# Performance work log

Hardware: AMD Instinct MI355X
Metric: run time of the kernel (lower is better)

Reference implementation:

```python
import jax, jax.numpy as jnp
import numpy as np

ALPHA = 0.1
B, T, D = 32, 1024, 384


def _build_alive(T):
    # Expert j (1-indexed) is created at time j with lifetime 2^(ctz(j)+2)+1.
    def lifetime(j):
        k = (j & -j).bit_length() - 1
        return 2 ** (k + 2) + 1

    sets = [[j for j in range(1, t + 1) if t < j + lifetime(j)]
            for t in range(1, T + 1)]
    K = max(len(s) for s in sets)
    # pad with sentinel index T (the extra never-consumed expert slot)
    idx = np.full((T, K), T, dtype=np.int32)
    mask = np.zeros((T, K), dtype=np.float32)
    for t0, s in enumerate(sets):
        for i, j in enumerate(s):
            idx[t0, i] = j - 1  # 0-indexed expert slot
            mask[t0, i] = 1.0
    return idx, mask


def setup_inputs() -> dict:
    key = jax.random.key(0)
    kx, kw, kb = jax.random.split(key, 3)
    n_exp = T + 1
    x = jax.random.normal(kx, (B, T, D), dtype=jnp.float32)
    # stand-in STULayer = Linear(D, D) per expert
    W = jax.random.normal(kw, (n_exp, D, D), dtype=jnp.float32) / np.float32(np.sqrt(D))
    b = jax.random.normal(kb, (n_exp, D), dtype=jnp.float32) * 0.02
    idx, mask = _build_alive(T)
    return {"x": x, "W": W, "b": b,
            "alive_idx": jnp.asarray(idx), "alive_mask": jnp.asarray(mask)}


def reference(x, W, b, alive_idx, alive_mask):
    Bb, Tt, Dd = x.shape
    n_exp = W.shape[0]
    # initial pool: 1 expert with weight 1
    p0 = jnp.zeros((n_exp,), x.dtype).at[0].set(1.0)
    new_idx = jnp.arange(1, Tt + 1, dtype=jnp.int32)      # slot of expert created at step t
    t_f = jnp.arange(1, Tt + 1, dtype=x.dtype)            # p[new] = 1/t

    def step(p, inp):
        x_t, idx, mask, ni, tf = inp          # x_t: [B,D]; idx,mask: [K]
        Wg = W[idx]                            # [K,D,D]
        bg = b[idx]                            # [K,D]
        outs = jnp.einsum('bd,kde->kbe', x_t, Wg) + bg[:, None, :]  # [K,B,D]
        p_a = p[idx] * mask                    # weights of alive experts
        w = p_a / jnp.sum(p_a)                 # normalized (torch keeps them pre-normalized)
        y_t = jnp.einsum('k,kbe->be', w, outs)
        # soft cross-entropy of expert outputs against x_t (ChunkedCrossEntropyLoss stand-in)
        tgt = jax.nn.softmax(x_t, axis=-1)                       # [B,D]
        logp = jax.nn.log_softmax(outs, axis=-1)                 # [K,B,D]
        loss = -jnp.mean(jnp.sum(tgt[None, :, :] * logp, axis=-1), axis=-1)  # [K]
        loss = jax.lax.stop_gradient(loss)     # torch uses .item() => detached
        # multiplicative weight update, normalize over alive set
        p_upd = p_a * jnp.exp(-ALPHA * loss) * mask
        p_upd = p_upd / jnp.sum(p_upd)
        p = p.at[idx].set(jnp.where(mask > 0, p_upd, p[idx]))
        # spawn new expert with weight 1/t (renormalization deferred to use time)
        p = p.at[ni].set(1.0 / tf)
        return p, y_t

    xs = (jnp.swapaxes(x, 0, 1), alive_idx, alive_mask, new_idx, t_f)
    _, ys = jax.lax.scan(step, p0, xs)        # ys: [T,B,D]
    return jnp.swapaxes(ys, 0, 1)
```

## Files before the change

### kernel.cpp

```cpp
#include <hip/hip_runtime.h>

#define TT 1024
#define BB 32
#define DD 384
#define NE 1025
#define ALPHA_ 0.1f
#define TC 4
#define KSTEP 64
#define NKS 6
#define MROWS 128
#define PADK 72
#define NTHR 512

typedef __attribute__((ext_vector_type(8))) short short8;
typedef __attribute__((ext_vector_type(8))) unsigned short ushort8;
typedef __attribute__((ext_vector_type(4))) float f32x4;

__device__ __forceinline__ unsigned short f2bf(float f) {
    unsigned int u = __float_as_uint(f);
    unsigned int r = u + 0x7fffu + ((u >> 16) & 1u);
    return (unsigned short)(r >> 16);
}

__device__ __host__ __forceinline__ int chunks_of(int j, int* Lout) {
    int k = __builtin_ctz(j);
    int life = (1 << (k + 2)) + 1;
    int jend = j + life - 1; if (jend > TT) jend = TT;
    int L = jend - j + 1;
    *Lout = L;
    return (L + TC - 1) / TC;
}

__device__ __forceinline__ void gl16(const void* g, void* l) {
    __builtin_amdgcn_global_load_lds(
        (const __attribute__((address_space(1))) void*)g,
        (__attribute__((address_space(3))) void*)l, 16, 0, 0);
}

__device__ __forceinline__ float dppsum32(float v) {
    float t;
    t = __int_as_float(__builtin_amdgcn_update_dpp(0, __float_as_int(v), 0x111, 0xf, 0xf, true)); v += t;
    t = __int_as_float(__builtin_amdgcn_update_dpp(0, __float_as_int(v), 0x112, 0xf, 0xf, true)); v += t;
    t = __int_as_float(__builtin_amdgcn_update_dpp(0, __float_as_int(v), 0x114, 0xf, 0xf, true)); v += t;
    t = __int_as_float(__builtin_amdgcn_update_dpp(0, __float_as_int(v), 0x118, 0xf, 0xf, true)); v += t;
    t = __int_as_float(__builtin_amdgcn_update_dpp(0, __float_as_int(v), 0x142, 0xf, 0xf, true)); v += t;
    return __int_as_float(__builtin_amdgcn_readlane(__float_as_int(v), 31));
}

__global__ void setup_all(int* __restrict__ table, int* __restrict__ pref,
                          short* __restrict__ perm16,
                          const int* __restrict__ aidx, const float* __restrict__ amask,
                          int K) {
    __shared__ int sc[1024];
    int b = blockIdx.x, t = threadIdx.x;
    if (b == 0) {
        int j = t + 1;
        int L; int nc = chunks_of(j, &L);
        int start = 0;
        for (int jp = 1; jp < j; ++jp) { int Lp; start += chunks_of(jp, &Lp); }
        for (int c = 0; c < nc; ++c) {
            int cnt = L - c * TC; if (cnt > TC) cnt = TC;
            int* e = table + 3 * (start + c);
            e[0] = j - 1;
            e[1] = (j - 1) + c * TC;
            e[2] = cnt;
        }
    } else if (b == 1) {
        int c = 0;
        for (int kk = 0; kk < K; ++kk) c += (amask[t * K + kk] > 0.f) ? 1 : 0;
        sc[t] = c;
        __syncthreads();
        for (int off = 1; off < 1024; off <<= 1) {
            int v = (t >= off) ? sc[t - off] : 0;
            __syncthreads();
            sc[t] += v;
            __syncthreads();
        }
        if (t == 0) pref[0] = 0;
        pref[t + 1] = sc[t];
    } else {
        int t0 = b - 2;
        int l = t;
        if (l < 32) {
            short enc = 63;
            if (t0 >= 1 && t0 <= TT - 1 && l < K && amask[t0 * K + l] > 0.f) {
                int sp = aidx[t0 * K + l];
                if (sp == t0) enc = (short)(-sp);
                else {
                    for (int kk = 0; kk < K; ++kk)
                        if (aidx[(t0 - 1) * K + kk] == sp) { enc = (short)kk; break; }
                }
            }
            perm16[t0 * 32 + l] = enc;
        }
    }
}

__global__ __launch_bounds__(512)
void conv_w2(const float* __restrict__ W, unsigned short* __restrict__ Wperm) {
    int db = blockIdx.x;
    int j  = blockIdx.y;
    int tid = threadIdx.x, l = tid & 63, w8 = tid >> 6;
    const float* Wj = W + (size_t)j * (DD * DD)
                        + (size_t)(db * 32 + (l >> 4) * 8) * DD + (l & 15);
#pragma unroll
    for (int it = 0; it < 3; ++it) {
        int eblk = it * 8 + w8;
        const float* src = Wj + eblk * 16;
        ushort8 h;
#pragma unroll
        for (int k = 0; k < 8; ++k) h[k] = f2bf(src[(size_t)k * DD]);
        *(ushort8*)&Wperm[(((size_t)j * 12 + db) * 24 + eblk) * 512 + l * 8] = h;
    }
}

__global__ __launch_bounds__(512)
void conv_x2(const float* __restrict__ x, unsigned short* __restrict__ xperm) {
    int t = blockIdx.x;
    int tid = threadIdx.x, l = tid & 63, w8 = tid >> 6;
#pragma unroll
    for (int it = 0; it < 3; ++it) {
        int T = it * 8 + w8;
        int bb = T / 12, db = T - bb * 12;
        const float* src = x + ((size_t)(bb * 16 + (l & 15)) * TT + t) * DD
                             + db * 32 + (l >> 4) * 8;
        float4 f0 = *(const float4*)src;
        float4 f1 = *(const float4*)(src + 4);
        ushort8 h;
        h[0] = f2bf(f0.x); h[1] = f2bf(f0.y); h[2] = f2bf(f0.z); h[3] = f2bf(f0.w);
        h[4] = f2bf(f1.x); h[5] = f2bf(f1.y); h[6] = f2bf(f1.z); h[7] = f2bf(f1.w);
        *(ushort8*)&xperm[(size_t)t * 12288 + T * 512 + l * 8] = h;
    }
}

__global__ void conv_tgt(const float* __restrict__ x, unsigned short* __restrict__ tgtbf) {
    __shared__ unsigned short sL[8 * 384];
    int tid = threadIdx.x;
    int wid = tid >> 6, lane = tid & 63;
    size_t row = (size_t)blockIdx.x * 8 + wid;
    const float* xr = x + row * DD;
    float v[6]; float m = -1e30f;
#pragma unroll
    for (int i = 0; i < 6; ++i) { v[i] = xr[lane + 64 * i]; m = fmaxf(m, v[i]); }
#pragma unroll
    for (int d = 1; d < 64; d <<= 1) m = fmaxf(m, __shfl_xor(m, d));
    float s = 0.f;
#pragma unroll
    for (int i = 0; i < 6; ++i) { v[i] = __expf(v[i] - m); s += v[i]; }
#pragma unroll
    for (int d = 1; d < 64; d <<= 1) s += __shfl_xor(s, d);
    float rz = 1.0f / s;
#pragma unroll
    for (int i = 0; i < 6; ++i) sL[wid * 384 + lane + 64 * i] = f2bf(v[i] * rz);
    __syncthreads();
    unsigned int* dst = (unsigned int*)(tgtbf + (size_t)blockIdx.x * 8 * 384);
    const unsigned int* s32 = (const unsigned int*)sL;
#pragma unroll
    for (int i = 0; i < 3; ++i) dst[i * 512 + tid] = s32[i * 512 + tid];
}

__global__ __launch_bounds__(1024)
void gemmA(const unsigned short* __restrict__ xperm,
           const unsigned short* __restrict__ Wperm,
           const float* __restrict__ bias,
           const int* __restrict__ aidx,
           const unsigned short* __restrict__ tgtbf,
           float* __restrict__ Epad,
           const int* __restrict__ table, int nblk, int K,
           const int* __restrict__ pref,
           unsigned short* __restrict__ outs)
{
    __shared__ __align__(16) unsigned short sA[2][4096];
    __shared__ __align__(16) unsigned short sB[2][12288];
    __shared__ float sRow[128];
    __shared__ int sKK[TC];
    __shared__ int sSlot[TC];

    int bid = blockIdx.x;
    int q8 = nblk >> 3, r8 = nblk & 7;
    int xcd = bid & 7, pos = bid >> 3;
    int lb = (xcd < r8 ? xcd * (q8 + 1) : r8 * (q8 + 1) + (xcd - r8) * q8) + pos;

    int s = table[3 * lb], t0s = table[3 * lb + 1], cnt = table[3 * lb + 2];

    int tid = threadIdx.x;
    int wid = tid >> 6, lane = tid & 63;
    int waveM = wid >> 2, waveN = wid & 3;
    int lc = lane & 15, lg = lane >> 4;

    int tcl[4];
#pragma unroll
    for (int tc = 0; tc < 4; ++tc) { int t = t0s + tc; tcl[tc] = t > TT - 1 ? TT - 1 : t; }

    f32x4 acc[2][6];
    f32x4 zz = {0.f, 0.f, 0.f, 0.f};
#pragma unroll
    for (int m = 0; m < 2; ++m)
#pragma unroll
        for (int n = 0; n < 6; ++n) acc[m][n] = zz;

    const size_t wbase = (size_t)s * (12 * 24 * 512);

    auto stage = [&](int buf, int ks) {
        if (wid < 8) {
            int tc = wid >> 1, bb = wid & 1;
            const unsigned short* asrc = xperm + ((size_t)tcl[tc] * 24 + bb * 12 + ks) * 512 + lane * 8;
            gl16(asrc, &sA[buf][wid * 512]);
            const unsigned short* bsrc = Wperm + wbase + ((size_t)ks * 24 + 16 + wid) * 512 + lane * 8;
            gl16(bsrc, &sB[buf][(16 + wid) * 512]);
        } else {
            int e0 = (wid - 8) * 2;
            const unsigned short* b0 = Wperm + wbase + ((size_t)ks * 24 + e0) * 512 + lane * 8;
            gl16(b0, &sB[buf][e0 * 512]);
            gl16(b0 + 512, &sB[buf][(e0 + 1) * 512]);
        }
    };

    stage(0, 0);
    stage(1, 1);
    for (int ks = 0; ks < 12; ++ks) {
        int cur = ks & 1;
        if (ks < 11) asm volatile("s_waitcnt vmcnt(2)" ::: "memory");
        else         asm volatile("s_waitcnt vmcnt(0)" ::: "memory");
        __builtin_amdgcn_s_barrier();
        __builtin_amdgcn_sched_barrier(0);
        short8 af[2], bfr[6];
#pragma unroll
        for (int mf = 0; mf < 2; ++mf)
            af[mf] = *(const short8*)&sA[cur][(waveM * 2 + mf) * 512 + lane * 8];
#pragma unroll
        for (int nf = 0; nf < 6; ++nf)
            bfr[nf] = *(const short8*)&sB[cur][(waveN * 6 + nf) * 512 + lane * 8];
        __builtin_amdgcn_s_setprio(1);
#pragma unroll
        for (int mf = 0; mf < 2; ++mf)
#pragma unroll
            for (int nf = 0; nf < 6; ++nf)
                acc[mf][nf] = __builtin_amdgcn_mfma_f32_16x16x32_bf16(af[mf], bfr[nf], acc[mf][nf], 0, 0, 0);
        __builtin_amdgcn_s_setprio(0);
        __builtin_amdgcn_sched_barrier(0);
        __builtin_amdgcn_s_barrier();
        __builtin_amdgcn_sched_barrier(0);
        if (ks < 10) stage(cur, ks + 2);
    }
    __syncthreads();

    float* sStat = (float*)&sA[0][0];
    if (tid < TC) {
        int kk = 0, slot = 0;
        if (tid < cnt) {
            int t = t0s + tid;
            for (int k2 = 0; k2 < K; ++k2)
                if (aidx[t * K + k2] == s) { kk = k2; break; }
            if (pref) slot = pref[t] + kk;
        }
        sKK[tid] = kk;
        sSlot[tid] = slot;
    }
#pragma unroll
    for (int nf = 0; nf < 6; ++nf) {
        float be = bias[(size_t)s * DD + waveN * 96 + nf * 16 + lc];
#pragma unroll
        for (int mf = 0; mf < 2; ++mf)
#pragma unroll
            for (int rr = 0; rr < 4; ++rr) acc[mf][nf][rr] += be;
    }
#pragma unroll
    for (int mf = 0; mf < 2; ++mf)
#pragma unroll
        for (int rr = 0; rr < 4; ++rr) {
            float m = acc[mf][0][rr];
#pragma unroll
            for (int nf = 1; nf < 6; ++nf) m = fmaxf(m, acc[mf][nf][rr]);
#pragma unroll
            for (int d = 1; d < 16; d <<= 1) m = fmaxf(m, __shfl_xor(m, d));
            if (lc == 0) sStat[(waveM * 32 + mf * 16 + lg * 4 + rr) * 12 + waveN] = m;
        }
    __syncthreads();
    if (outs && waveM < cnt) {
        unsigned short* ob = outs + (size_t)sSlot[waveM] * 12288;
#pragma unroll
        for (int mf = 0; mf < 2; ++mf)
#pragma unroll
            for (int nf = 0; nf < 6; ++nf) {
                int c2 = mf * 24 + waveN * 6 + nf;
                unsigned int lo, hi;
                asm("v_cvt_pk_bf16_f32 %0, %1, %2" : "=v"(lo)
                    : "v"(acc[mf][nf][0]), "v"(acc[mf][nf][1]));
                asm("v_cvt_pk_bf16_f32 %0, %1, %2" : "=v"(hi)
                    : "v"(acc[mf][nf][2]), "v"(acc[mf][nf][3]));
                uint2 pk; pk.x = lo; pk.y = hi;
                *(uint2*)&ob[c2 * 256 + lane * 4] = pk;
            }
    }
#pragma unroll
    for (int mf = 0; mf < 2; ++mf)
#pragma unroll
        for (int rr = 0; rr < 4; ++rr) {
            int row = waveM * 32 + mf * 16 + lg * 4 + rr;
            const f32x4 pm = *(const f32x4*)&sStat[row * 12];
            float rmax = fmaxf(fmaxf(pm[0], pm[1]), fmaxf(pm[2], pm[3]));
            int tcr = row >> 5, b = row & 31;
            int t = tcl[tcr];
            const unsigned short* tg = tgtbf + ((size_t)b * TT + t) * DD;
            float psum = 0.f, pdot = 0.f;
#pragma unroll
            for (int nf = 0; nf < 6; ++nf) {
                int e = waveN * 96 + nf * 16 + lc;
                float a = acc[mf][nf][rr];
                psum += __expf(a - rmax);
                float tv = __uint_as_float(((unsigned int)tg[e]) << 16);
                pdot += tv * a;
            }
#pragma unroll
            for (int d = 1; d < 16; d <<= 1) { psum += __shfl_xor(psum, d); pdot += __shfl_xor(pdot, d); }
            if (lc == 0) { sStat[row * 12 + 4 + waveN] = psum; sStat[row * 12 + 8 + waveN] = pdot; }
        }
    __syncthreads();
    if (wid == 0) {
#pragma unroll
        for (int h = 0; h < 2; ++h) {
            int row = lane + h * 64;
            const f32x4 mm = *(const f32x4*)&sStat[row * 12];
            const f32x4 pp = *(const f32x4*)&sStat[row * 12 + 4];
            const f32x4 dd = *(const f32x4*)&sStat[row * 12 + 8];
            float rmax = fmaxf(fmaxf(mm[0], mm[1]), fmaxf(mm[2], mm[3]));
            float S = pp[0] + pp[1] + pp[2] + pp[3];
            float Dt = dd[0] + dd[1] + dd[2] + dd[3];
            sRow[row] = rmax + logf(S) - Dt;
        }
    }
    __syncthreads();
    if (wid == 0) {
#pragma unroll
        for (int pph = 0; pph < 2; ++pph) {
            int tc = pph * 2 + (lane >> 5);
            int b = lane & 31;
            float v = (tc < cnt) ? sRow[tc * 32 + b] : 0.f;
#pragma unroll
            for (int d = 1; d < 32; d <<= 1) v += __shfl_xor(v, d);
            if (b == 0 && tc < cnt) {
                float loss = v * (1.0f / 32.0f);
                float E = expf(-ALPHA_ * loss);
                int t0 = t0s + tc;
                Epad[t0 * 32 + sKK[tc]] = E;
            }
        }
    }
}

__global__ __launch_bounds__(256)
void recur3(const float* __restrict__ Epad, const short* __restrict__ perm16,
            const int* __restrict__ aidx, const float* __restrict__ amask,
            float* __restrict__ wraw, int K) {
    __shared__ __align__(16) float sE[2][4096];
    __shared__ __align__(16) short sP[2][4160];
    int tid = threadIdx.x, wid = tid >> 6, lane = tid & 63;
    int l = lane;

    auto stageCh = [&](int buf, int c) {
        const float* eb = Epad + c * 4096;
#pragma unroll
        for (int i = wid; i < 16; i += 4)
            gl16(eb + i * 256 + lane * 4, &sE[buf][i * 256]);
        const short* pb = perm16 + (c * 128 + 1) * 32;
#pragma unroll
        for (int i = wid; i < 8; i += 4)
            gl16(pb + i * 512 + lane * 8, &sP[buf][32 + i * 512]);
    };

    stageCh(0, 0);
    __syncthreads();

    float pr = 0.f;
    if (l < K && amask[l] > 0.f && aidx[l] == 0) pr = 1.f;

    int buf = 0;
    for (int c = 0; c < 8; ++c) {
        if (c < 7) stageCh(buf ^ 1, c + 1);
        if (wid == 0) {
            float curE = (l < 32) ? sE[buf][l] : 0.f;
            short curP = (l < 32) ? sP[buf][32 + l] : (short)63;
            for (int tl = 0; tl < 128; ++tl) {
                float nE = 0.f; short nP = 63;
                if (tl < 127) {
                    nE = sE[buf][(tl + 1) * 32 + (l & 31)];
                    nP = sP[buf][(tl + 2) * 32 + (l & 31)];
                }
                int t = c * 128 + tl;
                if (l < 32) wraw[t * 32 + l] = pr;
                float qv = pr * curE;
                float S2 = dppsum32(qv);
                float pn = qv / S2;
                int pe = (l < 32) ? (int)curP : 63;
                int src = pe >= 0 ? pe : 0;
                float sv = __shfl(pn, src);
                pr = (pe >= 0) ? sv : (1.0f / (float)(-pe));
                curE = (l < 32) ? nE : 0.f;
                curP = nP;
            }
        }
        __syncthreads();
        buf ^= 1;
    }
}

__global__ void wnorm(float* __restrict__ w) {
    int tid = threadIdx.x;
    int wid = tid >> 6, lane = tid & 63;
    int half = lane >> 5, l = lane & 31;
    int t = blockIdx.x * 8 + wid * 2 + half;
    float v = w[t * 32 + l];
    float s = v;
#pragma unroll
    for (int d = 1; d < 32; d <<= 1) s += __shfl_xor(s, d);
    w[t * 32 + l] = v / s;
}

__global__ __launch_bounds__(512)
void mixout(const unsigned short* __restrict__ outs, const float* __restrict__ wts32,
            const int* __restrict__ pref, float* __restrict__ y) {
    int t = blockIdx.x;
    __shared__ float sW[32];
    int tid = threadIdx.x;
    if (tid < 32) sW[tid] = wts32[t * 32 + tid];
    __syncthreads();
    int p0 = pref[t];
    int L = pref[t + 1] - p0;
    float acc[24];
#pragma unroll
    for (int i = 0; i < 24; ++i) acc[i] = 0.f;
    const ushort8* base = (const ushort8*)(outs + (size_t)p0 * 12288);
    for (int kk = 0; kk < L; ++kk) {
        float w = sW[kk];
        const ushort8* sp = base + (size_t)kk * 1536;
#pragma unroll
        for (int pass = 0; pass < 3; ++pass) {
            ushort8 v = sp[pass * 512 + tid];
#pragma unroll
            for (int j = 0; j < 8; ++j)
                acc[pass * 8 + j] += w * __uint_as_float(((unsigned int)v[j]) << 16);
        }
    }
#pragma unroll
    for (int pass = 0; pass < 3; ++pass) {
        int idx = pass * 512 + tid;
        int c2 = idx >> 5;
        int lane0 = (idx * 2) & 63;
        int mf = (c2 >= 24) ? 1 : 0;
        int rem = c2 - mf * 24;
        int wN = rem / 6, nf = rem - wN * 6;
        int e0 = wN * 96 + nf * 16 + (lane0 & 15);
        int bb = mf * 16 + (lane0 >> 4) * 4;
#pragma unroll
        for (int r = 0; r < 4; ++r) {
            int b = bb + r;
            float2 st;
            st.x = acc[pass * 8 + r];
            st.y = acc[pass * 8 + 4 + r];
            *(float2*)&y[((size_t)b * TT + t) * DD + e0] = st;
        }
    }
}

__global__ void setup_blocks(int* __restrict__ table) {
    int j = threadIdx.x + 1;
    int L; int nc = chunks_of(j, &L);
    int start = 0;
    for (int jp = 1; jp < j; ++jp) { int Lp; start += chunks_of(jp, &Lp); }
    for (int c = 0; c < nc; ++c) {
        int cnt = L - c * TC; if (cnt > TC) cnt = TC;
        int* e = table + 3 * (start + c);
        e[0] = j - 1;
        e[1] = (j - 1) + c * TC;
        e[2] = cnt;
    }
}

__global__ void setup_union(int* __restrict__ uCount, int* __restrict__ uList) {
    int c = threadIdx.x;
    int t1 = 2 * c + 1, t2 = 2 * c + 2;
    int n = 0;
    for (int j = 1; j <= t2 && j <= TT; ++j) {
        int k = __builtin_ctz(j);
        int life = (1 << (k + 2)) + 1;
        if (j + life - 1 >= t1) { if (n < 32) uList[c * 32 + n] = j - 1; n++; }
    }
    uCount[c] = n > 32 ? 32 : n;
}

__global__ void setup_perm3(const int* __restrict__ aidx, const float* __restrict__ amask,
                            short* __restrict__ perm16, int K) {
    int t0 = blockIdx.x;
    int l = threadIdx.x;
    short enc = 63;
    if (t0 >= 1 && t0 <= TT - 1 && l < K && amask[t0 * K + l] > 0.f) {
        int sp = aidx[t0 * K + l];
        if (sp == t0) enc = (short)(-sp);
        else {
            for (int kk = 0; kk < K; ++kk)
                if (aidx[(t0 - 1) * K + kk] == sp) { enc = (short)kk; break; }
        }
    }
    perm16[t0 * 32 + l] = enc;
}

__global__ void conv_w(const float* __restrict__ W, unsigned short* __restrict__ Wperm) {
    int db = blockIdx.x;
    int j  = blockIdx.y;
    __shared__ __align__(16) unsigned short sL[12288];
    int tid = threadIdx.x;
    int r = tid >> 4, q = tid & 15;
    const float* src = W + (size_t)j * (DD * DD) + (size_t)(db * 32 + r) * DD + q * 24;
#pragma unroll
    for (int i = 0; i < 6; ++i) {
        float4 f = *(const float4*)(src + i * 4);
        int e0 = q * 24 + i * 4;
        float fv[4] = {f.x, f.y, f.z, f.w};
#pragma unroll
        for (int m = 0; m < 4; ++m) {
            int e = e0 + m;
            int off = (e >> 4) * 512 + (r >> 3) * 128 + (e & 15) * 8 + (r & 7);
            sL[off] = f2bf(fv[m]);
        }
    }
    __syncthreads();
    ushort8* dst = (ushort8*)(Wperm + ((size_t)j * 12 + db) * 12288);
    const ushort8* s8 = (const ushort8*)sL;
#pragma unroll
    for (int i = 0; i < 3; ++i) dst[tid * 3 + i] = s8[tid * 3 + i];
}

__global__ void conv_x(const float* __restrict__ x, unsigned short* __restrict__ xperm) {
    int t = blockIdx.x;
    __shared__ __align__(16) unsigned short sL[12288];
    int tid = threadIdx.x;
    int b = tid >> 4, q = tid & 15;
    const float* src = x + ((size_t)b * TT + t) * DD + q * 24;
#pragma unroll
    for (int i = 0; i < 6; ++i) {
        float4 f = *(const float4*)(src + i * 4);
        int d0 = q * 24 + i * 4;
        float fv[4] = {f.x, f.y, f.z, f.w};
#pragma unroll
        for (int m = 0; m < 4; ++m) {
            int d = d0 + m;
            int off = ((b >> 4) * 12 + (d >> 5)) * 512 + ((d >> 3) & 3) * 128 + (b & 15) * 8 + (d & 7);
            sL[off] = f2bf(fv[m]);
        }
    }
    __syncthreads();
    ushort8* dst = (ushort8*)(xperm + (size_t)t * 12288);
    const ushort8* s8 = (const ushort8*)sL;
#pragma unroll
    for (int i = 0; i < 3; ++i) dst[tid * 3 + i] = s8[tid * 3 + i];
}

__global__ __launch_bounds__(1024)
void gemmC(const unsigned short* __restrict__ xperm,
           const unsigned short* __restrict__ Wperm,
           const float* __restrict__ bias,
           const int* __restrict__ aidx,
           const float* __restrict__ wts32,
           const int* __restrict__ uCount, const int* __restrict__ uList,
           float* __restrict__ y, int K)
{
    __shared__ __align__(16) unsigned short sAF[24576];
    __shared__ __align__(16) unsigned short sB[2][12288];
    __shared__ float sWu[64];
    __shared__ int   sUL[32];
    __shared__ float sBv[768];

    int nb = gridDim.x;
    int bid = blockIdx.x;
    int q8 = nb >> 3, r8 = nb & 7;
    int xcd = bid & 7, pos = bid >> 3;
    int c = (xcd < r8 ? xcd * (q8 + 1) : r8 * (q8 + 1) + (xcd - r8) * q8) + pos;

    int t0 = c * 2;
    int tid = threadIdx.x, wid = tid >> 6, lane = tid & 63;
    int waveM = wid >> 2, waveN = wid & 3;
    int lc = lane & 15, lg = lane >> 4;
    int tcw = waveM >> 1, bbw = waveM & 1;

    int uc = uCount[c];
    if (tid < uc) sUL[tid] = uList[c * 32 + tid];
#pragma unroll
    for (int i = 0; i < 3; ++i) {
        int T = wid * 3 + i;
        int tc = T / 24, bb = (T / 12) & 1, db = T % 12;
        const unsigned short* src = xperm + ((size_t)(t0 + tc) * 24 + bb * 12 + db) * 512 + lane * 8;
        gl16(src, &sAF[T * 512]);
    }
    __syncthreads();
    if (tid < 2 * uc) {
        int u = tid >> 1, tc = tid & 1;
        int j = sUL[u];
        float wv = 0.f;
        for (int kk = 0; kk < K; ++kk)
            if (aidx[(t0 + tc) * K + kk] == j) { wv = wts32[(t0 + tc) * 32 + kk]; break; }
        sWu[u * 2 + tc] = wv;
    }
    __syncthreads();
    {
        size_t wb = (size_t)sUL[0] * (12 * 24 * 512);
        const unsigned short* b0 = Wperm + wb + (size_t)wid * 512 + lane * 8;
        gl16(b0, &sB[0][wid * 512]);
        if (wid < 8) {
            const unsigned short* b1 = Wperm + wb + (size_t)(16 + wid) * 512 + lane * 8;
            gl16(b1, &sB[0][(16 + wid) * 512]);
        }
    }
    for (int i = tid; i < 768; i += 1024) {
        int tc = (i >= 384) ? 1 : 0; int e = i - tc * 384;
        float a = 0.f;
        for (int u = 0; u < uc; ++u) a += sWu[u * 2 + tc] * bias[(size_t)sUL[u] * DD + e];
        sBv[i] = a;
    }
    __syncthreads();

    f32x4 accY[6], accE[6];
    f32x4 zz = {0.f, 0.f, 0.f, 0.f};
#pragma unroll
    for (int n = 0; n < 6; ++n) { accY[n] = zz; accE[n] = zz; }

    int buf = 0;
    for (int u = 0; u < uc; ++u) {
        float wv = sWu[u * 2 + tcw];
        bool act = (wv != 0.f);
        for (int ks = 0; ks < 12; ++ks) {
            int nu = u, nk = ks + 1;
            if (nk == 12) { nk = 0; nu = u + 1; }
            if (nu < uc) {
                size_t wb = (size_t)sUL[nu] * (12 * 24 * 512) + (size_t)nk * (24 * 512);
                const unsigned short* b0 = Wperm + wb + (size_t)wid * 512 + lane * 8;
                gl16(b0, &sB[buf ^ 1][wid * 512]);
                if (wid < 8) {
                    const unsigned short* b1 = Wperm + wb + (size_t)(16 + wid) * 512 + lane * 8;
                    gl16(b1, &sB[buf ^ 1][(16 + wid) * 512]);
                }
            }
            if (act) {
                short8 af = *(const short8*)&sAF[(waveM * 12 + ks) * 512 + lane * 8];
#pragma unroll
                for (int nf = 0; nf < 6; ++nf) {
                    short8 bf = *(const short8*)&sB[buf][(waveN * 6 + nf) * 512 + lane * 8];
                    accE[nf] = __builtin_amdgcn_mfma_f32_16x16x32_bf16(af, bf, accE[nf], 0, 0, 0);
                }
            }
            __syncthreads();
            buf ^= 1;
        }
        if (act) {
#pragma unroll
            for (int nf = 0; nf < 6; ++nf)
#pragma unroll
                for (int rr = 0; rr < 4; ++rr) { accY[nf][rr] += wv * accE[nf][rr]; accE[nf][rr] = 0.f; }
        }
    }

    int t = t0 + tcw;
#pragma unroll
    for (int nf = 0; nf < 6; ++nf) {
        int e = waveN * 96 + nf * 16 + lc;
        float bvv = sBv[tcw * 384 + e];
#pragma unroll
        for (int rr = 0; rr < 4; ++rr) {
            int b = bbw * 16 + lg * 4 + rr;
            y[((size_t)b * TT + t) * DD + e] = accY[nf][rr] + bvv;
        }
    }
}

__global__ void rowstats(const float* __restrict__ x, float* __restrict__ xm,
                         float* __restrict__ rz) {
    int wid = threadIdx.x >> 6;
    int lane = threadIdx.x & 63;
    int row = blockIdx.x * 4 + wid;
    const float* xr = x + (size_t)row * DD;
    float v[6];
    float m = -1e30f;
#pragma unroll
    for (int i = 0; i < 6; ++i) { v[i] = xr[lane + 64 * i]; m = fmaxf(m, v[i]); }
#pragma unroll
    for (int d = 1; d < 64; d <<= 1) m = fmaxf(m, __shfl_xor(m, d));
    float s = 0.f;
#pragma unroll
    for (int i = 0; i < 6; ++i) s += expf(v[i] - m);
#pragma unroll
    for (int d = 1; d < 64; d <<= 1) s += __shfl_xor(s, d);
    if (lane == 0) { xm[row] = m; rz[row] = 1.0f / s; }
}

template<int MODE>
__global__ __launch_bounds__(NTHR)
void gemm_phase(const float* __restrict__ x, const float* __restrict__ W,
                const float* __restrict__ bias, const int* __restrict__ aidx,
                const float* __restrict__ xm, const float* __restrict__ rz,
                const float* __restrict__ wts, float* __restrict__ Earr,
                float* __restrict__ y, const int* __restrict__ table,
                int nblk, int K)
{
    __shared__ __align__(16) unsigned short sA[MROWS * PADK];
    __shared__ __align__(16) unsigned short sB[DD * PADK];
    __shared__ float sRow[MROWS];
    __shared__ float sCoef[TC];

    int bid = blockIdx.x;
    int q = nblk >> 3, r = nblk & 7;
    int xcd = bid & 7, pos = bid >> 3;
    int lb = (xcd < r ? xcd * (q + 1) : r * (q + 1) + (xcd - r) * q) + pos;

    int s = table[3 * lb], t0s = table[3 * lb + 1], cnt = table[3 * lb + 2];

    int tid = threadIdx.x;
    int wid = tid >> 6, lane = tid & 63;
    int waveM = wid >> 2, waveN = wid & 3;
    int lc = lane & 15, lg = lane >> 4;

    if (MODE == 1 && tid < TC) {
        float c = 0.f;
        if (tid < cnt) {
            int t0 = t0s + tid;
            for (int kk = 0; kk < K; ++kk)
                if (aidx[t0 * K + kk] == s) { c = wts[t0 * K + kk]; break; }
        }
        sCoef[tid] = c;
    }

    f32x4 acc[4][6];
    f32x4 zz = {0.f, 0.f, 0.f, 0.f};
#pragma unroll
    for (int i = 0; i < 4; ++i)
#pragma unroll
        for (int n = 0; n < 6; ++n) acc[i][n] = zz;

    const float* Wj = W + (size_t)s * (DD * DD);

    int xr = tid >> 2, xq = tid & 3;
    int xtc = xr >> 5, xb = xr & 31;
    int xt = t0s + xtc; if (xt > TT - 1) xt = TT - 1;
    const float* xrow = x + ((size_t)xb * TT + xt) * DD;

    for (int ks = 0; ks < NKS; ++ks) {
        const int d0 = ks * KSTEP;
        __syncthreads();
        {
            const float4* src = (const float4*)(xrow + d0 + xq * 16);
            float4 f0 = src[0], f1 = src[1], f2 = src[2], f3 = src[3];
            short8 v0, v1;
            v0[0] = (short)f2bf(f0.x); v0[1] = (short)f2bf(f0.y);
            v0[2] = (short)f2bf(f0.z); v0[3] = (short)f2bf(f0.w);
            v0[4] = (short)f2bf(f1.x); v0[5] = (short)f2bf(f1.y);
            v0[6] = (short)f2bf(f1.z); v0[7] = (short)f2bf(f1.w);
            v1[0] = (short)f2bf(f2.x); v1[1] = (short)f2bf(f2.y);
            v1[2] = (short)f2bf(f2.z); v1[3] = (short)f2bf(f2.w);
            v1[4] = (short)f2bf(f3.x); v1[5] = (short)f2bf(f3.y);
            v1[6] = (short)f2bf(f3.z); v1[7] = (short)f2bf(f3.w);
            short8* dst = (short8*)&sA[xr * PADK + xq * 16];
            dst[0] = v0; dst[1] = v1;
        }
        {
            int dbase = d0 + wid * 8;
#pragma unroll
            for (int g = 0; g < 6; ++g) {
                int e = g * 64 + lane;
                const float* col = Wj + (size_t)dbase * DD + e;
                short8 h;
#pragma unroll
                for (int dd = 0; dd < 8; ++dd) h[dd] = (short)f2bf(col[(size_t)dd * DD]);
                *(short8*)&sB[e * PADK + wid * 8] = h;
            }
        }
        __syncthreads();
#pragma unroll
        for (int kh = 0; kh < 2; ++kh) {
            short8 af[4], bfr[6];
#pragma unroll
            for (int mf = 0; mf < 4; ++mf)
                af[mf] = *(const short8*)&sA[(waveM * 64 + mf * 16 + lc) * PADK + kh * 32 + lg * 8];
#pragma unroll
            for (int nf = 0; nf < 6; ++nf)
                bfr[nf] = *(const short8*)&sB[(waveN * 96 + nf * 16 + lc) * PADK + kh * 32 + lg * 8];
#pragma unroll
            for (int mf = 0; mf < 4; ++mf)
#pragma unroll
                for (int nf = 0; nf < 6; ++nf)
                    acc[mf][nf] = __builtin_amdgcn_mfma_f32_16x16x32_bf16(af[mf], bfr[nf], acc[mf][nf], 0, 0, 0);
        }
    }

    if (MODE == 0) {
        __syncthreads();
        float* sStat = (float*)sA;
#pragma unroll
        for (int nf = 0; nf < 6; ++nf) {
            float be = bias[(size_t)s * DD + waveN * 96 + nf * 16 + lc];
#pragma unroll
            for (int mf = 0; mf < 4; ++mf)
#pragma unroll
                for (int rr = 0; rr < 4; ++rr) acc[mf][nf][rr] += be;
        }
#pragma unroll
        for (int mf = 0; mf < 4; ++mf)
#pragma unroll
            for (int rr = 0; rr < 4; ++rr) {
                float m = acc[mf][0][rr];
#pragma unroll
                for (int nf = 1; nf < 6; ++nf) m = fmaxf(m, acc[mf][nf][rr]);
#pragma unroll
                for (int d = 1; d < 16; d <<= 1) m = fmaxf(m, __shfl_xor(m, d));
                if (lc == 0) sStat[(waveM * 64 + mf * 16 + lg * 4 + rr) * 12 + waveN] = m;
            }
        __syncthreads();
#pragma unroll
        for (int mf = 0; mf < 4; ++mf)
#pragma unroll
            for (int rr = 0; rr < 4; ++rr) {
                int row = waveM * 64 + mf * 16 + lg * 4 + rr;
                const f32x4 pm = *(const f32x4*)&sStat[row * 12];
                float rmax = fmaxf(fmaxf(pm[0], pm[1]), fmaxf(pm[2], pm[3]));
                int tc = row >> 5, b = row & 31;
                int t = t0s + tc; if (t > TT - 1) t = TT - 1;
                float xmv = xm[b * TT + t];
                float rzv = rz[b * TT + t];
                const float* x2 = x + ((size_t)b * TT + t) * DD;
                float psum = 0.f, pdot = 0.f;
#pragma unroll
                for (int nf = 0; nf < 6; ++nf) {
                    int e = waveN * 96 + nf * 16 + lc;
                    float a = acc[mf][nf][rr];
                    psum += __expf(a - rmax);
                    float tg = __expf(x2[e] - xmv) * rzv;
                    pdot += tg * a;
                }
#pragma unroll
                for (int d = 1; d < 16; d <<= 1) {
                    psum += __shfl_xor(psum, d);
                    pdot += __shfl_xor(pdot, d);
                }
                if (lc == 0) { sStat[row * 12 + 4 + waveN] = psum; sStat[row * 12 + 8 + waveN] = pdot; }
            }
        __syncthreads();
        if (wid == 0) {
#pragma unroll
            for (int h = 0; h < 2; ++h) {
                int row = lane + h * 64;
                const f32x4 mm = *(const f32x4*)&sStat[row * 12];
                const f32x4 pp = *(const f32x4*)&sStat[row * 12 + 4];
                const f32x4 dd = *(const f32x4*)&sStat[row * 12 + 8];
                float rmax = fmaxf(fmaxf(mm[0], mm[1]), fmaxf(mm[2], mm[3]));
                float S = pp[0] + pp[1] + pp[2] + pp[3];
                float Dt = dd[0] + dd[1] + dd[2] + dd[3];
                sRow[row] = rmax + logf(S) - Dt;
            }
        }
        __syncthreads();
        if (wid == 0) {
#pragma unroll
            for (int pph = 0; pph < 2; ++pph) {
                int tc = pph * 2 + (lane >> 5);
                int b = lane & 31;
                float v = (tc < cnt) ? sRow[tc * 32 + b] : 0.f;
#pragma unroll
                for (int d = 1; d < 32; d <<= 1) v += __shfl_xor(v, d);
                if (b == 0 && tc < cnt) {
                    float loss = v * (1.0f / 32.0f);
                    float E = expf(-ALPHA_ * loss);
                    int t0 = t0s + tc;
                    for (int kk = 0; kk < K; ++kk)
                        if (aidx[t0 * K + kk] == s) { Earr[t0 * K + kk] = E; break; }
                }
            }
        }
    } else {
#pragma unroll
        for (int mf = 0; mf < 4; ++mf)
#pragma unroll
            for (int rr = 0; rr < 4; ++rr) {
                int row = waveM * 64 + mf * 16 + lg * 4 + rr;
                int tc = row >> 5, b = row & 31;
                if (tc < cnt) {
                    float c = sCoef[tc];
                    int t = t0s + tc;
                    float* yr = y + ((size_t)b * TT + t) * DD + waveN * 96 + lc;
#pragma unroll
                    for (int nf = 0; nf < 6; ++nf)
                        atomicAdd(yr + nf * 16, c * acc[mf][nf][rr]);
                }
            }
    }
}

__global__ void recurrence(const int* __restrict__ aidx, const float* __restrict__ amask,
                           const float* __restrict__ Earr, float* __restrict__ wts, int K) {
    __shared__ float p[NE];
    int l = threadIdx.x;
    for (int i = l; i < NE; i += 64) p[i] = 0.f;
    __syncthreads();
    if (l == 0) p[0] = 1.f;
    __syncthreads();

    int idxv = TT; float mv = 0.f, Ev = 1.f;
    if (l < K) { idxv = aidx[l]; mv = amask[l]; Ev = Earr[l]; }

    for (int t0 = 0; t0 < TT; ++t0) {
        int idxn = TT; float mn = 0.f, En = 1.f;
        if (t0 + 1 < TT && l < K) {
            idxn = aidx[(t0 + 1) * K + l];
            mn = amask[(t0 + 1) * K + l];
            En = Earr[(t0 + 1) * K + l];
        }
        float pa = (l < K) ? p[idxv] * mv : 0.f;
        float qv = pa * Ev;
        float S1 = pa, S2 = qv;
#pragma unroll
        for (int d = 1; d < 64; d <<= 1) {
            S1 += __shfl_xor(S1, d);
            S2 += __shfl_xor(S2, d);
        }
        float w = pa / S1;
        if (l < K) wts[t0 * K + l] = w;
        float pn = qv / S2;
        __syncthreads();
        if (l < K && mv > 0.f) p[idxv] = pn;
        if (l == 0) p[t0 + 1] = 1.0f / (float)(t0 + 1);
        __syncthreads();
        idxv = idxn; mv = mn; Ev = En;
    }
}

__global__ void bias_init(const float* __restrict__ bias, const int* __restrict__ aidx,
                          const float* __restrict__ wts, float* __restrict__ y, int K) {
    int t0 = blockIdx.x;
    int e = threadIdx.x;
    float acc = 0.f;
    for (int kk = 0; kk < K; ++kk) {
        float w = wts[t0 * K + kk];
        int s = aidx[t0 * K + kk];
        acc += w * bias[(size_t)s * DD + e];
    }
    for (int b = 0; b < BB; ++b)
        y[((size_t)b * TT + t0) * DD + e] = acc;
}

extern "C" void kernel_launch(void* const* d_in, const int* in_sizes, int n_in,
                              void* d_out, int out_size, void* d_ws, size_t ws_size,
                              hipStream_t stream) {
    const float* x = (const float*)d_in[0];
    const float* W = (const float*)d_in[1];
    const float* bv = (const float*)d_in[2];
    const int* aidx = (const int*)d_in[3];
    const float* amask = (const float*)d_in[4];
    float* y = (float*)d_out;
    const int K = in_sizes[3] / TT;

    int nblk = 0, NSLOT = 0;
    for (int j = 1; j <= TT; ++j) { int L; nblk += chunks_of(j, &L); NSLOT += L; }

    size_t szW = (size_t)1024 * 294912;
    size_t szX = (size_t)1024 * 24576;
    size_t szT = (size_t)BB * TT * DD * 2;
    size_t szEp = (size_t)TT * 32 * sizeof(float);
    size_t szWt = (size_t)TT * 32 * sizeof(float);
    size_t szPm = (size_t)(TT + 1) * 32 * sizeof(short);
    size_t szTab = (size_t)6144 * 3 * sizeof(int);
    size_t szUC = 512 * sizeof(int);
    size_t szUL = 512 * 32 * sizeof(int);
    size_t szO  = (size_t)NSLOT * 12288 * 2;
    size_t szPf = (size_t)(TT + 1) * sizeof(int);
    size_t need2 = szW + szX + szT + szEp + szWt + szPm + szTab + szUC + szUL + 256;
    size_t need1 = need2 + szO + szPf;

    if (ws_size >= need1) {
        unsigned char* p = (unsigned char*)d_ws;
        unsigned short* Wperm = (unsigned short*)p; p += szW;
        unsigned short* xperm = (unsigned short*)p; p += szX;
        unsigned short* tgtb  = (unsigned short*)p; p += szT;
        float* Epad = (float*)p; p += szEp;
        float* wts32 = (float*)p; p += szWt;
        short* perm16 = (short*)p; p += szPm;
        int* table  = (int*)p;   p += szTab;
        int* uCnt   = (int*)p;   p += szUC;
        int* uLst   = (int*)p;   p += szUL;
        int* pref   = (int*)p;   p += szPf;
        unsigned short* outs = (unsigned short*)p; p += szO;

        hipLaunchKernelGGL(setup_all, dim3(TT + 3), dim3(1024), 0, stream,
                           table, pref, perm16, aidx, amask, K);
        hipLaunchKernelGGL(conv_w2, dim3(12, 1024), dim3(512), 0, stream, W, Wperm);
        hipLaunchKernelGGL(conv_x2, dim3(TT), dim3(512), 0, stream, x, xperm);
        hipLaunchKernelGGL(conv_tgt, dim3(BB * TT / 8), dim3(512), 0, stream, x, tgtb);
        hipMemsetAsync(Epad, 0, szEp, stream);
        hipLaunchKernelGGL(gemmA, dim3(nblk), dim3(1024), 0, stream,
                           xperm, Wperm, bv, aidx, tgtb, Epad, table, nblk, K, pref, outs);
        hipLaunchKernelGGL(recur3, dim3(1), dim3(256), 0, stream,
                           Epad, perm16, aidx, amask, wts32, K);
        hipLaunchKernelGGL(wnorm, dim3(TT / 8), dim3(256), 0, stream, wts32);
        hipLaunchKernelGGL(mixout, dim3(TT), dim3(512), 0, stream, outs, wts32, pref, y);
    } else if (ws_size >= need2) {
        unsigned char* p = (unsigned char*)d_ws;
        unsigned short* Wperm = (unsigned short*)p; p += szW;
        unsigned short* xperm = (unsigned short*)p; p += szX;
        unsigned short* tgtb  = (unsigned short*)p; p += szT;
        float* Epad = (float*)p; p += szEp;
        float* wts32 = (float*)p; p += szWt;
        short* perm16 = (short*)p; p += szPm;
        int* table  = (int*)p;   p += szTab;
        int* uCnt   = (int*)p;   p += szUC;
        int* uLst   = (int*)p;   p += szUL;

        hipLaunchKernelGGL(setup_blocks, dim3(1), dim3(1024), 0, stream, table);
        hipLaunchKernelGGL(setup_union, dim3(1), dim3(512), 0, stream, uCnt, uLst);
        hipLaunchKernelGGL(setup_perm3, dim3(TT + 1), dim3(32), 0, stream, aidx, amask, perm16, K);
        hipLaunchKernelGGL(conv_w, dim3(12, 1024), dim3(512), 0, stream, W, Wperm);
        hipLaunchKernelGGL(conv_x, dim3(TT), dim3(512), 0, stream, x, xperm);
        hipLaunchKernelGGL(conv_tgt, dim3(BB * TT / 8), dim3(512), 0, stream, x, tgtb);
        hipMemsetAsync(Epad, 0, szEp, stream);
        hipLaunchKernelGGL(gemmA, dim3(nblk), dim3(1024), 0, stream,
                           xperm, Wperm, bv, aidx, tgtb, Epad, table, nblk, K,
                           (const int*)nullptr, (unsigned short*)nullptr);
        hipLaunchKernelGGL(recur3, dim3(1), dim3(256), 0, stream,
                           Epad, perm16, aidx, amask, wts32, K);
        hipLaunchKernelGGL(wnorm, dim3(TT / 8), dim3(256), 0, stream, wts32);
        hipLaunchKernelGGL(gemmC, dim3(512), dim3(1024), 0, stream,
                           xperm, Wperm, bv, aidx, wts32, uCnt, uLst, y, K);
    } else {
        float* Earr = (float*)d_ws;
        float* wts = Earr + (size_t)TT * K;
        float* xm = wts + (size_t)TT * K;
        float* rz = xm + (size_t)BB * TT;
        int* table = (int*)(rz + (size_t)BB * TT);

        hipLaunchKernelGGL(setup_blocks, dim3(1), dim3(1024), 0, stream, table);
        hipLaunchKernelGGL(rowstats, dim3(BB * TT / 4), dim3(256), 0, stream, x, xm, rz);
        hipLaunchKernelGGL((gemm_phase<0>), dim3(nblk), dim3(NTHR), 0, stream,
                           x, W, bv, aidx, xm, rz, (const float*)nullptr, Earr,
                           (float*)nullptr, table, nblk, K);
        hipLaunchKernelGGL(recurrence, dim3(1), dim3(64), 0, stream, aidx, amask, Earr, wts, K);
        hipLaunchKernelGGL(bias_init, dim3(TT), dim3(DD), 0, stream, bv, aidx, wts, y, K);
        hipLaunchKernelGGL((gemm_phase<1>), dim3(nblk), dim3(NTHR), 0, stream,
                           x, W, bv, aidx, xm, rz, wts, (float*)nullptr, y, table, nblk, K);
    }
}
```

Before: 1.064 ms.

## Halve gemmA block to 512 threads with four M-fragments per wave

The gemmA block shrinks from 16 waves to 8. Each wave now computes a 64x96 tile (4 M-fragments by 6 N-fragments) instead of 32x96. Staging is redistributed so each wave issues four 16-byte global-to-LDS loads, the vmcnt wait depth is raised to match, and B fragments are loaded one at a time and reused across the four A fragments. This cuts redundant LDS reads of B and lowers barrier and thread overhead, at the cost of twice the accumulator registers per wave and fewer waves to hide latency.

```diff
diff --git a/kernel.cpp b/kernel.cpp
--- a/kernel.cpp
+++ b/kernel.cpp
@@ -159,7 +159,7 @@
     for (int i = 0; i < 3; ++i) dst[i * 512 + tid] = s32[i * 512 + tid];
 }
 
-__global__ __launch_bounds__(1024)
+__global__ __launch_bounds__(512)
 void gemmA(const unsigned short* __restrict__ xperm,
            const unsigned short* __restrict__ Wperm,
            const float* __restrict__ bias,
@@ -192,27 +192,28 @@
 #pragma unroll
     for (int tc = 0; tc < 4; ++tc) { int t = t0s + tc; tcl[tc] = t > TT - 1 ? TT - 1 : t; }
 
-    f32x4 acc[2][6];
+    f32x4 acc[4][6];
     f32x4 zz = {0.f, 0.f, 0.f, 0.f};
 #pragma unroll
-    for (int m = 0; m < 2; ++m)
+    for (int m = 0; m < 4; ++m)
 #pragma unroll
         for (int n = 0; n < 6; ++n) acc[m][n] = zz;
 
     const size_t wbase = (size_t)s * (12 * 24 * 512);
 
     auto stage = [&](int buf, int ks) {
-        if (wid < 8) {
-            int tc = wid >> 1, bb = wid & 1;
-            const unsigned short* asrc = xperm + ((size_t)tcl[tc] * 24 + bb * 12 + ks) * 512 + lane * 8;
-            gl16(asrc, &sA[buf][wid * 512]);
-            const unsigned short* bsrc = Wperm + wbase + ((size_t)ks * 24 + 16 + wid) * 512 + lane * 8;
-            gl16(bsrc, &sB[buf][(16 + wid) * 512]);
-        } else {
-            int e0 = (wid - 8) * 2;
-            const unsigned short* b0 = Wperm + wbase + ((size_t)ks * 24 + e0) * 512 + lane * 8;
-            gl16(b0, &sB[buf][e0 * 512]);
-            gl16(b0 + 512, &sB[buf][(e0 + 1) * 512]);
+#pragma unroll
+        for (int i = 0; i < 4; ++i) {
+            int T = wid * 4 + i;
+            if (T < 8) {
+                int tc = T >> 1, bb = T & 1;
+                const unsigned short* asrc = xperm + ((size_t)tcl[tc] * 24 + bb * 12 + ks) * 512 + lane * 8;
+                gl16(asrc, &sA[buf][T * 512]);
+            } else {
+                int eb = T - 8;
+                const unsigned short* bsrc = Wperm + wbase + ((size_t)ks * 24 + eb) * 512 + lane * 8;
+                gl16(bsrc, &sB[buf][eb * 512]);
+            }
         }
     };
 
@@ -220,23 +221,22 @@
     stage(1, 1);
     for (int ks = 0; ks < 12; ++ks) {
         int cur = ks & 1;
-        if (ks < 11) asm volatile("s_waitcnt vmcnt(2)" ::: "memory");
+        if (ks < 11) asm volatile("s_waitcnt vmcnt(4)" ::: "memory");
         else         asm volatile("s_waitcnt vmcnt(0)" ::: "memory");
         __builtin_amdgcn_s_barrier();
         __builtin_amdgcn_sched_barrier(0);
-        short8 af[2], bfr[6];
-#pragma unroll
-        for (int mf = 0; mf < 2; ++mf)
-            af[mf] = *(const short8*)&sA[cur][(waveM * 2 + mf) * 512 + lane * 8];
-#pragma unroll
-        for (int nf = 0; nf < 6; ++nf)
-            bfr[nf] = *(const short8*)&sB[cur][(waveN * 6 + nf) * 512 + lane * 8];
+        short8 af[4];
+#pragma unroll
+        for (int mf = 0; mf < 4; ++mf)
+            af[mf] = *(const short8*)&sA[cur][(waveM * 4 + mf) * 512 + lane * 8];
         __builtin_amdgcn_s_setprio(1);
 #pragma unroll
-        for (int mf = 0; mf < 2; ++mf)
-#pragma unroll
-            for (int nf = 0; nf < 6; ++nf)
-                acc[mf][nf] = __builtin_amdgcn_mfma_f32_16x16x32_bf16(af[mf], bfr[nf], acc[mf][nf], 0, 0, 0);
+        for (int nf = 0; nf < 6; ++nf) {
+            short8 bf = *(const short8*)&sB[cur][(waveN * 6 + nf) * 512 + lane * 8];
+#pragma unroll
+            for (int mf = 0; mf < 4; ++mf)
+                acc[mf][nf] = __builtin_amdgcn_mfma_f32_16x16x32_bf16(af[mf], bf, acc[mf][nf], 0, 0, 0);
+        }
         __builtin_amdgcn_s_setprio(0);
         __builtin_amdgcn_sched_barrier(0);
         __builtin_amdgcn_s_barrier();
@@ -261,12 +261,12 @@
     for (int nf = 0; nf < 6; ++nf) {
         float be = bias[(size_t)s * DD + waveN * 96 + nf * 16 + lc];
 #pragma unroll
-        for (int mf = 0; mf < 2; ++mf)
+        for (int mf = 0; mf < 4; ++mf)
 #pragma unroll
             for (int rr = 0; rr < 4; ++rr) acc[mf][nf][rr] += be;
     }
 #pragma unroll
-    for (int mf = 0; mf < 2; ++mf)
+    for (int mf = 0; mf < 4; ++mf)
 #pragma unroll
         for (int rr = 0; rr < 4; ++rr) {
             float m = acc[mf][0][rr];
@@ -274,30 +274,34 @@
             for (int nf = 1; nf < 6; ++nf) m = fmaxf(m, acc[mf][nf][rr]);
 #pragma unroll
             for (int d = 1; d < 16; d <<= 1) m = fmaxf(m, __shfl_xor(m, d));
-            if (lc == 0) sStat[(waveM * 32 + mf * 16 + lg * 4 + rr) * 12 + waveN] = m;
-        }
-    __syncthreads();
-    if (outs && waveM < cnt) {
-        unsigned short* ob = outs + (size_t)sSlot[waveM] * 12288;
-#pragma unroll
-        for (int mf = 0; mf < 2; ++mf)
-#pragma unroll
-            for (int nf = 0; nf < 6; ++nf) {
-                int c2 = mf * 24 + waveN * 6 + nf;
-                unsigned int lo, hi;
-                asm("v_cvt_pk_bf16_f32 %0, %1, %2" : "=v"(lo)
-                    : "v"(acc[mf][nf][0]), "v"(acc[mf][nf][1]));
-                asm("v_cvt_pk_bf16_f32 %0, %1, %2" : "=v"(hi)
-                    : "v"(acc[mf][nf][2]), "v"(acc[mf][nf][3]));
-                uint2 pk; pk.x = lo; pk.y = hi;
-                *(uint2*)&ob[c2 * 256 + lane * 4] = pk;
-            }
-    }
-#pragma unroll
-    for (int mf = 0; mf < 2; ++mf)
+            if (lc == 0) sStat[(waveM * 64 + mf * 16 + lg * 4 + rr) * 12 + waveN] = m;
+        }
+    __syncthreads();
+    if (outs) {
+#pragma unroll
+        for (int mf = 0; mf < 4; ++mf) {
+            int tcr = waveM * 2 + (mf >> 1);
+            if (tcr < cnt) {
+                unsigned short* ob = outs + (size_t)sSlot[tcr] * 12288;
+#pragma unroll
+                for (int nf = 0; nf < 6; ++nf) {
+                    int c2 = (mf & 1) * 24 + waveN * 6 + nf;
+                    unsigned int lo, hi;
+                    asm("v_cvt_pk_bf16_f32 %0, %1, %2" : "=v"(lo)
+                        : "v"(acc[mf][nf][0]), "v"(acc[mf][nf][1]));
+                    asm("v_cvt_pk_bf16_f32 %0, %1, %2" : "=v"(hi)
+                        : "v"(acc[mf][nf][2]), "v"(acc[mf][nf][3]));
+                    uint2 pk; pk.x = lo; pk.y = hi;
+                    *(uint2*)&ob[c2 * 256 + lane * 4] = pk;
+                }
+            }
+        }
+    }
+#pragma unroll
+    for (int mf = 0; mf < 4; ++mf)
 #pragma unroll
         for (int rr = 0; rr < 4; ++rr) {
-            int row = waveM * 32 + mf * 16 + lg * 4 + rr;
+            int row = waveM * 64 + mf * 16 + lg * 4 + rr;
             const f32x4 pm = *(const f32x4*)&sStat[row * 12];
             float rmax = fmaxf(fmaxf(pm[0], pm[1]), fmaxf(pm[2], pm[3]));
             int tcr = row >> 5, b = row & 31;
@@ -992,7 +996,7 @@
         hipLaunchKernelGGL(conv_x2, dim3(TT), dim3(512), 0, stream, x, xperm);
         hipLaunchKernelGGL(conv_tgt, dim3(BB * TT / 8), dim3(512), 0, stream, x, tgtb);
         hipMemsetAsync(Epad, 0, szEp, stream);
-        hipLaunchKernelGGL(gemmA, dim3(nblk), dim3(1024), 0, stream,
+        hipLaunchKernelGGL(gemmA, dim3(nblk), dim3(512), 0, stream,
                            xperm, Wperm, bv, aidx, tgtb, Epad, table, nblk, K, pref, outs);
         hipLaunchKernelGGL(recur3, dim3(1), dim3(256), 0, stream,
                            Epad, perm16, aidx, amask, wts32, K);
@@ -1017,7 +1021,7 @@
         hipLaunchKernelGGL(conv_x, dim3(TT), dim3(512), 0, stream, x, xperm);
         hipLaunchKernelGGL(conv_tgt, dim3(BB * TT / 8), dim3(512), 0, stream, x, tgtb);
         hipMemsetAsync(Epad, 0, szEp, stream);
-        hipLaunchKernelGGL(gemmA, dim3(nblk), dim3(1024), 0, stream,
+        hipLaunchKernelGGL(gemmA, dim3(nblk), dim3(512), 0, stream,
                            xperm, Wperm, bv, aidx, tgtb, Epad, table, nblk, K,
                            (const int*)nullptr, (unsigned short*)nullptr);
         hipLaunchKernelGGL(recur3, dim3(1), dim3(256), 0, stream,
```

After: 1.098 ms. 3.2% more time.
